# Kernel optimization log

Hardware: AMD Instinct MI355X
Metric: run time of the kernel (lower is better)

Reference implementation:

```python
import jax, jax.numpy as jnp
import numpy as np

B_SZ, SEQ, H, P = 4, 8192, 512, 256


def _s5(x, lam_re, lam_im, log_dt, b_re, b_im, c_re, c_im, d):
    """Single-direction S5 diagonal SSM. x: [B,L,H] -> y: [B,L,H]."""
    lam = lam_re + 1j * lam_im                      # [P] complex diagonal A
    dt = jnp.exp(log_dt)                            # [P] ZOH timestep
    a_bar = jnp.exp(lam * dt)                       # [P] discretized A
    b_bar = ((a_bar - 1.0) / lam)[:, None] * (b_re + 1j * b_im)  # [P,H]
    bu = jnp.einsum('blh,ph->blp', x.astype(b_bar.dtype), b_bar)  # [B,L,P]
    a_el = jnp.broadcast_to(a_bar, bu.shape)        # time-invariant A per step

    def comb(e1, e2):  # associative combine for linear recurrence
        a1, s1 = e1
        a2, s2 = e2
        return (a1 * a2, a2 * s1 + s2)

    _, states = jax.lax.associative_scan(comb, (a_el, bu), axis=1)  # [B,L,P]
    c = c_re + 1j * c_im                            # [H,P]
    return jnp.einsum('blp,hp->blh', states, c).real + x * d


def setup_inputs() -> dict:
    key = jax.random.key(0)
    ks = jax.random.split(key, 10)
    return {
        'x': jax.random.normal(ks[0], (B_SZ, SEQ, H), dtype=jnp.float32),
        'Lambda_re': -0.1 - 0.5 * jax.random.uniform(ks[1], (2, P), dtype=jnp.float32),
        'Lambda_im': jnp.pi * jax.random.normal(ks[2], (2, P), dtype=jnp.float32),
        'log_dt': jnp.log(0.001) + (jnp.log(0.1) - jnp.log(0.001)) * jax.random.uniform(ks[3], (2, P), dtype=jnp.float32),
        'B_re': jax.random.normal(ks[4], (2, P, H), dtype=jnp.float32) / np.sqrt(H),
        'B_im': jax.random.normal(ks[5], (2, P, H), dtype=jnp.float32) / np.sqrt(H),
        'C_re': jax.random.normal(ks[6], (2, H, P), dtype=jnp.float32) / np.sqrt(P),
        'C_im': jax.random.normal(ks[7], (2, H, P), dtype=jnp.float32) / np.sqrt(P),
        'D': jax.random.normal(ks[8], (2, H), dtype=jnp.float32),
    }


def reference(x, Lambda_re, Lambda_im, log_dt, B_re, B_im, C_re, C_im, D):
    # fwd(x) + flip(bwd(flip(x)))
    y_f = _s5(x, Lambda_re[0], Lambda_im[0], log_dt[0], B_re[0], B_im[0], C_re[0], C_im[0], D[0])
    x_r = x[:, ::-1]
    y_b = _s5(x_r, Lambda_re[1], Lambda_im[1], log_dt[1], B_re[1], B_im[1], C_re[1], C_im[1], D[1])[:, ::-1]
    return y_f + y_b
```

## Files before the change

### kernel.cpp

```cpp
#include <hip/hip_runtime.h>
#include <math.h>

typedef unsigned short ushort_t;
typedef __bf16 bf16x8 __attribute__((ext_vector_type(8)));
typedef ushort_t ushort8v __attribute__((ext_vector_type(8)));
typedef float f32x4 __attribute__((ext_vector_type(4)));

#define B_SZ   4
#define SEQ    8192
#define M_ROWS (B_SZ * SEQ)
#define CH     128
#define NC     (SEQ / CH)

__device__ __forceinline__ ushort_t f2bf(float f) {
    unsigned u = __float_as_uint(f);
    u = u + 0x7fffu + ((u >> 16) & 1u);
    return (ushort_t)(u >> 16);
}
__device__ __forceinline__ float bf2f(ushort_t b) {
    return __uint_as_float(((unsigned)b) << 16);
}

__device__ __forceinline__ void load16_lds(const void* g, void* l) {
    __builtin_amdgcn_global_load_lds(
        (const __attribute__((address_space(1))) unsigned int*)g,
        (__attribute__((address_space(3))) unsigned int*)l, 16, 0, 0);
}

__global__ void param_kernel(const float* __restrict__ Lre,
                             const float* __restrict__ Lim,
                             const float* __restrict__ ldt,
                             float* __restrict__ abar,
                             float* __restrict__ apow,
                             float* __restrict__ coef) {
    int d = blockIdx.x, p = threadIdx.x;
    int ip = d * 256 + p;
    float lr = Lre[ip], li = Lim[ip];
    float dt = expf(ldt[ip]);
    float e   = expf(lr * dt);
    float ang = li * dt;
    float ar = e * cosf(ang), ai = e * sinf(ang);
    float nr = ar - 1.0f, ni = ai;
    float den = lr * lr + li * li;
    float cr = (nr * lr + ni * li) / den;
    float ci = (ni * lr - nr * li) / den;
    int o = d * 512 + 2 * p;
    abar[o] = ar;  abar[o + 1] = ai;
    float eC = expf(lr * dt * (float)CH);
    float aC = ang * (float)CH;
    apow[o] = eC * cosf(aC);  apow[o + 1] = eC * sinf(aC);
    coef[o] = cr;  coef[o + 1] = ci;
}

__global__ void bmat_kernel(const float* __restrict__ Bre,
                            const float* __restrict__ Bim,
                            const float* __restrict__ coef,
                            ushort_t* __restrict__ Bmat) {
    int idx = blockIdx.x * 256 + threadIdx.x;
    int h = idx & 511;
    int p = (idx >> 9) & 255;
    int d = idx >> 17;
    float cr = coef[d * 512 + 2 * p], ci = coef[d * 512 + 2 * p + 1];
    float br = Bre[idx], bi = Bim[idx];
    Bmat[(d * 512 + p) * 512 + h]       = f2bf(cr * br - ci * bi);
    Bmat[(d * 512 + 256 + p) * 512 + h] = f2bf(cr * bi + ci * br);
}

__global__ void cmat_kernel(const float* __restrict__ Cre,
                            const float* __restrict__ Cim,
                            ushort_t* __restrict__ Cmat) {
    int idx = blockIdx.x * 256 + threadIdx.x;
    int p = idx & 255;
    int h = (idx >> 8) & 511;
    int d = idx >> 17;
    Cmat[(d * 512 + h) * 512 + p]       = f2bf(Cre[idx]);
    Cmat[(d * 512 + h) * 512 + 256 + p] = f2bf(-Cim[idx]);
}

__global__ void conv_x_kernel(const float* __restrict__ x,
                              ushort_t* __restrict__ X16) {
    int i = blockIdx.x * 256 + threadIdx.x;
    float4 v = ((const float4*)x)[i];
    ushort_t o[4] = {f2bf(v.x), f2bf(v.y), f2bf(v.z), f2bf(v.w)};
    *(uint2*)&X16[(size_t)i * 4] = *(const uint2*)o;
}

template<int EPI>
__global__ __launch_bounds__(256)
void gemm_mfma(const ushort_t* __restrict__ A, const ushort_t* __restrict__ Bm,
               ushort_t* __restrict__ Cb, float* __restrict__ Cf,
               const float* __restrict__ X, const float* __restrict__ Dv) {
    __shared__ ushort_t As[128 * 32];
    __shared__ ushort_t Bs[128 * 32];
    const int tid  = threadIdx.x;
    const int lane = tid & 63;
    const int wv   = tid >> 6;
    const int wrow = wv >> 1, wcol = wv & 1;
    const int l15  = lane & 15, lq = lane >> 4;
    const int m0 = blockIdx.y * 128;
    const int n0 = blockIdx.x * 128;

    f32x4 acc[4][4];
#pragma unroll
    for (int i = 0; i < 4; ++i)
#pragma unroll
        for (int j = 0; j < 4; ++j)
            acc[i][j] = (f32x4){0.f, 0.f, 0.f, 0.f};

    const int grow_l = lane >> 2;
    const int gk8    = (lane & 3) * 8;

    const ushort_t* aF = As + (wrow * 64 + l15) * 32 + lq * 8;
    const ushort_t* bF = Bs + (wcol * 64 + l15) * 32 + lq * 8;

    for (int kt = 0; kt < 512; kt += 32) {
        __syncthreads();
#pragma unroll
        for (int j = 0; j < 2; ++j) {
            const int r0 = j * 64 + wv * 16;
            load16_lds(&A[(size_t)(m0 + r0 + grow_l) * 512 + kt + gk8],
                       (void*)&As[r0 * 32]);
            load16_lds(&Bm[(size_t)(n0 + r0 + grow_l) * 512 + kt + gk8],
                       (void*)&Bs[r0 * 32]);
        }
        __syncthreads();

        bf16x8 af[4], bf[4];
#pragma unroll
        for (int mi = 0; mi < 4; ++mi) {
            union { ushort8v u; bf16x8 b; } cv;
            cv.u = *(const ushort8v*)(aF + mi * 512);
            af[mi] = cv.b;
        }
#pragma unroll
        for (int ni = 0; ni < 4; ++ni) {
            union { ushort8v u; bf16x8 b; } cv;
            cv.u = *(const ushort8v*)(bF + ni * 512);
            bf[ni] = cv.b;
        }
#pragma unroll
        for (int mi = 0; mi < 4; ++mi)
#pragma unroll
            for (int ni = 0; ni < 4; ++ni)
                acc[mi][ni] = __builtin_amdgcn_mfma_f32_16x16x32_bf16(
                    af[mi], bf[ni], acc[mi][ni], 0, 0, 0);
    }

#pragma unroll
    for (int mi = 0; mi < 4; ++mi) {
#pragma unroll
        for (int ni = 0; ni < 4; ++ni) {
            const int col = n0 + wcol * 64 + ni * 16 + l15;
            float dsum = 0.f;
            if (EPI == 1) dsum = Dv[col] + Dv[512 + col];
#pragma unroll
            for (int r = 0; r < 4; ++r) {
                const int row = m0 + wrow * 64 + mi * 16 + lq * 4 + r;
                const size_t idx = (size_t)row * 512 + col;
                float v = acc[mi][ni][r];
                if (EPI == 0) {
                    Cb[idx] = f2bf(v);
                } else if (EPI == 1) {
                    Cf[idx] = v + X[idx] * dsum;
                } else {
                    Cf[idx] += v;
                }
            }
        }
    }
}

template<int DIR>
__global__ __launch_bounds__(256)
void scan_carry(const ushort_t* __restrict__ S, const float* __restrict__ abar,
                float* __restrict__ carry) {
    int b = blockIdx.x, c = blockIdx.y, p = threadIdx.x;
    float ar = abar[2 * p], ai = abar[2 * p + 1];
    float sr = 0.f, si = 0.f;
    size_t base = ((size_t)b * SEQ + (size_t)c * CH) * 512;
    for (int ii = 0; ii < CH; ++ii) {
        int i = (DIR == 0) ? ii : (CH - 1 - ii);
        const ushort_t* r = S + base + (size_t)i * 512;
        float re = bf2f(r[p]), im = bf2f(r[256 + p]);
        float nr = fmaf(ar, sr, fmaf(-ai, si, re));
        float ni = fmaf(ar, si, fmaf(ai, sr, im));
        sr = nr; si = ni;
    }
    int o = (b * NC + c) * 512 + 2 * p;
    carry[o] = sr; carry[o + 1] = si;
}

template<int DIR>
__global__ void scan_comb(const float* __restrict__ carry,
                          float* __restrict__ init,
                          const float* __restrict__ apow) {
    int b = blockIdx.x, p = threadIdx.x;
    float pr = apow[2 * p], pi = apow[2 * p + 1];
    float sr = 0.f, si = 0.f;
    for (int cc = 0; cc < NC; ++cc) {
        int c = (DIR == 0) ? cc : (NC - 1 - cc);
        int o = (b * NC + c) * 512 + 2 * p;
        init[o] = sr; init[o + 1] = si;
        float cr = carry[o], ci = carry[o + 1];
        float nr = fmaf(pr, sr, fmaf(-pi, si, cr));
        float ni = fmaf(pr, si, fmaf(pi, sr, ci));
        sr = nr; si = ni;
    }
}

template<int DIR>
__global__ __launch_bounds__(256)
void scan_final(ushort_t* __restrict__ S, const float* __restrict__ abar,
                const float* __restrict__ init) {
    int b = blockIdx.x, c = blockIdx.y, p = threadIdx.x;
    float ar = abar[2 * p], ai = abar[2 * p + 1];
    int o = (b * NC + c) * 512 + 2 * p;
    float sr = init[o], si = init[o + 1];
    size_t base = ((size_t)b * SEQ + (size_t)c * CH) * 512;
    for (int ii = 0; ii < CH; ++ii) {
        int i = (DIR == 0) ? ii : (CH - 1 - ii);
        ushort_t* r = S + base + (size_t)i * 512;
        float re = bf2f(r[p]), im = bf2f(r[256 + p]);
        float nr = fmaf(ar, sr, fmaf(-ai, si, re));
        float ni = fmaf(ar, si, fmaf(ai, sr, im));
        sr = nr; si = ni;
        r[p] = f2bf(sr); r[256 + p] = f2bf(si);
    }
}

extern "C" void kernel_launch(void* const* d_in, const int* in_sizes, int n_in,
                              void* d_out, int out_size, void* d_ws, size_t ws_size,
                              hipStream_t stream) {
    const float* x   = (const float*)d_in[0];
    const float* Lre = (const float*)d_in[1];
    const float* Lim = (const float*)d_in[2];
    const float* ldt = (const float*)d_in[3];
    const float* Bre = (const float*)d_in[4];
    const float* Bim = (const float*)d_in[5];
    const float* Cre = (const float*)d_in[6];
    const float* Cim = (const float*)d_in[7];
    const float* Dv  = (const float*)d_in[8];
    float* y = (float*)d_out;
    char* ws = (char*)d_ws;

    ushort_t* X16  = (ushort_t*)(ws);
    ushort_t* SB16 = (ushort_t*)(ws + 33554432);
    ushort_t* Bm16 = (ushort_t*)(ws + 67108864);
    ushort_t* Cm16 = (ushort_t*)(ws + 68157440);
    float* abar  = (float*)(ws + 69206016);
    float* apow  = (float*)(ws + 69210112);
    float* coef  = (float*)(ws + 69214208);
    float* carry = (float*)(ws + 69218304);
    float* initb = (float*)(ws + 69742592);

    param_kernel<<<2, 256, 0, stream>>>(Lre, Lim, ldt, abar, apow, coef);
    bmat_kernel<<<1024, 256, 0, stream>>>(Bre, Bim, coef, Bm16);
    cmat_kernel<<<1024, 256, 0, stream>>>(Cre, Cim, Cm16);
    conv_x_kernel<<<16384, 256, 0, stream>>>(x, X16);

    dim3 gg(4, 256);
    dim3 gs(B_SZ, NC);

    gemm_mfma<0><<<gg, 256, 0, stream>>>(X16, Bm16, SB16, nullptr, nullptr, nullptr);
    scan_carry<0><<<gs, 256, 0, stream>>>(SB16, abar, carry);
    scan_comb<0><<<B_SZ, 256, 0, stream>>>(carry, initb, apow);
    scan_final<0><<<gs, 256, 0, stream>>>(SB16, abar, initb);
    gemm_mfma<1><<<gg, 256, 0, stream>>>(SB16, Cm16, nullptr, y, x, Dv);

    gemm_mfma<0><<<gg, 256, 0, stream>>>(X16, Bm16 + 262144, SB16, nullptr, nullptr, nullptr);
    scan_carry<1><<<gs, 256, 0, stream>>>(SB16, abar + 512, carry);
    scan_comb<1><<<B_SZ, 256, 0, stream>>>(carry, initb, apow + 512);
    scan_final<1><<<gs, 256, 0, stream>>>(SB16, abar + 512, initb);
    gemm_mfma<2><<<gg, 256, 0, stream>>>(SB16, Cm16 + 262144, nullptr, y, nullptr, nullptr);
}
```

Baseline: 328.9 us.

## Fuse both scan directions into single GEMM/scan passes with interleaved complex layout

Both directions now share one input-projection GEMM that produces an N=1024 interleaved re/im state matrix. Each scan kernel handles both directions with 512 threads, and a single K=1024 output GEMM replaces two output GEMMs plus the read-modify-write accumulation into y. The parameter, B-matrix and C-matrix prep kernels are merged into one, and GEMM blocks are remapped so that neighbouring M tiles land on the same XCD for L2 reuse. This removes launches, the second pass over x/y and the fp32 accumulate traffic, at the cost of a workspace twice as large and a reused carry/init region.

```diff
diff --git a/kernel.cpp b/kernel.cpp
--- a/kernel.cpp
+++ b/kernel.cpp
@@ -27,13 +27,21 @@
         (__attribute__((address_space(3))) unsigned int*)l, 16, 0, 0);
 }
 
-__global__ void param_kernel(const float* __restrict__ Lre,
-                             const float* __restrict__ Lim,
-                             const float* __restrict__ ldt,
-                             float* __restrict__ abar,
-                             float* __restrict__ apow,
-                             float* __restrict__ coef) {
-    int d = blockIdx.x, p = threadIdx.x;
+__global__ void prep_kernel(const float* __restrict__ Lre,
+                            const float* __restrict__ Lim,
+                            const float* __restrict__ ldt,
+                            const float* __restrict__ Bre,
+                            const float* __restrict__ Bim,
+                            const float* __restrict__ Cre,
+                            const float* __restrict__ Cim,
+                            float* __restrict__ abar,
+                            float* __restrict__ apow,
+                            ushort_t* __restrict__ Bmat,
+                            ushort_t* __restrict__ Cmat) {
+    int idx = blockIdx.x * 256 + threadIdx.x;
+    int h = idx & 511;
+    int p = (idx >> 9) & 255;
+    int d = idx >> 17;
     int ip = d * 256 + p;
     float lr = Lre[ip], li = Lim[ip];
     float dt = expf(ldt[ip]);
@@ -44,37 +52,21 @@
     float den = lr * lr + li * li;
     float cr = (nr * lr + ni * li) / den;
     float ci = (ni * lr - nr * li) / den;
-    int o = d * 512 + 2 * p;
-    abar[o] = ar;  abar[o + 1] = ai;
-    float eC = expf(lr * dt * (float)CH);
-    float aC = ang * (float)CH;
-    apow[o] = eC * cosf(aC);  apow[o + 1] = eC * sinf(aC);
-    coef[o] = cr;  coef[o + 1] = ci;
-}
-
-__global__ void bmat_kernel(const float* __restrict__ Bre,
-                            const float* __restrict__ Bim,
-                            const float* __restrict__ coef,
-                            ushort_t* __restrict__ Bmat) {
-    int idx = blockIdx.x * 256 + threadIdx.x;
-    int h = idx & 511;
-    int p = (idx >> 9) & 255;
-    int d = idx >> 17;
-    float cr = coef[d * 512 + 2 * p], ci = coef[d * 512 + 2 * p + 1];
     float br = Bre[idx], bi = Bim[idx];
-    Bmat[(d * 512 + p) * 512 + h]       = f2bf(cr * br - ci * bi);
-    Bmat[(d * 512 + 256 + p) * 512 + h] = f2bf(cr * bi + ci * br);
-}
-
-__global__ void cmat_kernel(const float* __restrict__ Cre,
-                            const float* __restrict__ Cim,
-                            ushort_t* __restrict__ Cmat) {
-    int idx = blockIdx.x * 256 + threadIdx.x;
-    int p = idx & 255;
-    int h = (idx >> 8) & 511;
-    int d = idx >> 17;
-    Cmat[(d * 512 + h) * 512 + p]       = f2bf(Cre[idx]);
-    Cmat[(d * 512 + h) * 512 + 256 + p] = f2bf(-Cim[idx]);
+    Bmat[(d * 512 + 2 * p) * 512 + h]     = f2bf(cr * br - ci * bi);
+    Bmat[(d * 512 + 2 * p + 1) * 512 + h] = f2bf(cr * bi + ci * br);
+    if (h == 0) {
+        int o = d * 512 + 2 * p;
+        abar[o] = ar;  abar[o + 1] = ai;
+        float eC = expf(lr * dt * (float)CH);
+        float aC = ang * (float)CH;
+        apow[o] = eC * cosf(aC);  apow[o + 1] = eC * sinf(aC);
+    }
+    int p2 = idx & 255;
+    int h2 = (idx >> 8) & 511;
+    int d2 = idx >> 17;
+    Cmat[h2 * 1024 + d2 * 512 + 2 * p2]     = f2bf(Cre[idx]);
+    Cmat[h2 * 1024 + d2 * 512 + 2 * p2 + 1] = f2bf(-Cim[idx]);
 }
 
 __global__ void conv_x_kernel(const float* __restrict__ x,
@@ -85,7 +77,7 @@
     *(uint2*)&X16[(size_t)i * 4] = *(const uint2*)o;
 }
 
-template<int EPI>
+template<int EPI, int KD_, int NT>
 __global__ __launch_bounds__(256)
 void gemm_mfma(const ushort_t* __restrict__ A, const ushort_t* __restrict__ Bm,
                ushort_t* __restrict__ Cb, float* __restrict__ Cf,
@@ -97,15 +89,22 @@
     const int wv   = tid >> 6;
     const int wrow = wv >> 1, wcol = wv & 1;
     const int l15  = lane & 15, lq = lane >> 4;
-    const int m0 = blockIdx.y * 128;
-    const int n0 = blockIdx.x * 128;
+
+    const int lin = blockIdx.x;
+    const int xcd = lin & 7;
+    const int j   = lin >> 3;
+    const int mt  = xcd * 32 + j / NT;
+    const int nt  = j % NT;
+    const int m0 = mt * 128;
+    const int n0 = nt * 128;
+    const int CN = NT * 128;
 
     f32x4 acc[4][4];
 #pragma unroll
     for (int i = 0; i < 4; ++i)
 #pragma unroll
-        for (int j = 0; j < 4; ++j)
-            acc[i][j] = (f32x4){0.f, 0.f, 0.f, 0.f};
+        for (int jj = 0; jj < 4; ++jj)
+            acc[i][jj] = (f32x4){0.f, 0.f, 0.f, 0.f};
 
     const int grow_l = lane >> 2;
     const int gk8    = (lane & 3) * 8;
@@ -113,19 +112,19 @@
     const ushort_t* aF = As + (wrow * 64 + l15) * 32 + lq * 8;
     const ushort_t* bF = Bs + (wcol * 64 + l15) * 32 + lq * 8;
 
-    for (int kt = 0; kt < 512; kt += 32) {
+    for (int kt = 0; kt < KD_; kt += 32) {
         __syncthreads();
 #pragma unroll
-        for (int j = 0; j < 2; ++j) {
-            const int r0 = j * 64 + wv * 16;
-            load16_lds(&A[(size_t)(m0 + r0 + grow_l) * 512 + kt + gk8],
+        for (int j2 = 0; j2 < 2; ++j2) {
+            const int r0 = j2 * 64 + wv * 16;
+            load16_lds(&A[(size_t)(m0 + r0 + grow_l) * KD_ + kt + gk8],
                        (void*)&As[r0 * 32]);
-            load16_lds(&Bm[(size_t)(n0 + r0 + grow_l) * 512 + kt + gk8],
+            load16_lds(&Bm[(size_t)(n0 + r0 + grow_l) * KD_ + kt + gk8],
                        (void*)&Bs[r0 * 32]);
         }
         __syncthreads();
 
-        bf16x8 af[4], bf[4];
+        bf16x8 af[4], bfr[4];
 #pragma unroll
         for (int mi = 0; mi < 4; ++mi) {
             union { ushort8v u; bf16x8 b; } cv;
@@ -136,14 +135,14 @@
         for (int ni = 0; ni < 4; ++ni) {
             union { ushort8v u; bf16x8 b; } cv;
             cv.u = *(const ushort8v*)(bF + ni * 512);
-            bf[ni] = cv.b;
+            bfr[ni] = cv.b;
         }
 #pragma unroll
         for (int mi = 0; mi < 4; ++mi)
 #pragma unroll
             for (int ni = 0; ni < 4; ++ni)
                 acc[mi][ni] = __builtin_amdgcn_mfma_f32_16x16x32_bf16(
-                    af[mi], bf[ni], acc[mi][ni], 0, 0, 0);
+                    af[mi], bfr[ni], acc[mi][ni], 0, 0, 0);
     }
 
 #pragma unroll
@@ -156,50 +155,49 @@
 #pragma unroll
             for (int r = 0; r < 4; ++r) {
                 const int row = m0 + wrow * 64 + mi * 16 + lq * 4 + r;
-                const size_t idx = (size_t)row * 512 + col;
-                float v = acc[mi][ni][r];
                 if (EPI == 0) {
-                    Cb[idx] = f2bf(v);
-                } else if (EPI == 1) {
-                    Cf[idx] = v + X[idx] * dsum;
+                    Cb[(size_t)row * CN + col] = f2bf(acc[mi][ni][r]);
                 } else {
-                    Cf[idx] += v;
+                    const size_t idx = (size_t)row * 512 + col;
+                    Cf[idx] = acc[mi][ni][r] + X[idx] * dsum;
                 }
             }
         }
     }
 }
 
-template<int DIR>
-__global__ __launch_bounds__(256)
+__global__ __launch_bounds__(512)
 void scan_carry(const ushort_t* __restrict__ S, const float* __restrict__ abar,
                 float* __restrict__ carry) {
-    int b = blockIdx.x, c = blockIdx.y, p = threadIdx.x;
-    float ar = abar[2 * p], ai = abar[2 * p + 1];
+    int b = blockIdx.x, c = blockIdx.y, t = threadIdx.x;
+    int dir = t >> 8, p = t & 255;
+    float ar = abar[dir * 512 + 2 * p], ai = abar[dir * 512 + 2 * p + 1];
     float sr = 0.f, si = 0.f;
-    size_t base = ((size_t)b * SEQ + (size_t)c * CH) * 512;
+    const ushort_t* base = S + ((size_t)b * SEQ + (size_t)c * CH) * 1024
+                             + dir * 512 + 2 * p;
     for (int ii = 0; ii < CH; ++ii) {
-        int i = (DIR == 0) ? ii : (CH - 1 - ii);
-        const ushort_t* r = S + base + (size_t)i * 512;
-        float re = bf2f(r[p]), im = bf2f(r[256 + p]);
+        int i = dir ? (CH - 1 - ii) : ii;
+        unsigned u = *(const unsigned*)(base + (size_t)i * 1024);
+        float re = bf2f((ushort_t)(u & 0xffffu));
+        float im = bf2f((ushort_t)(u >> 16));
         float nr = fmaf(ar, sr, fmaf(-ai, si, re));
         float ni = fmaf(ar, si, fmaf(ai, sr, im));
         sr = nr; si = ni;
     }
-    int o = (b * NC + c) * 512 + 2 * p;
+    int o = (b * NC + c) * 1024 + dir * 512 + 2 * p;
     carry[o] = sr; carry[o + 1] = si;
 }
 
-template<int DIR>
-__global__ void scan_comb(const float* __restrict__ carry,
-                          float* __restrict__ init,
-                          const float* __restrict__ apow) {
-    int b = blockIdx.x, p = threadIdx.x;
-    float pr = apow[2 * p], pi = apow[2 * p + 1];
+__global__ __launch_bounds__(512)
+void scan_comb(const float* __restrict__ carry, float* __restrict__ init,
+               const float* __restrict__ apow) {
+    int b = blockIdx.x, t = threadIdx.x;
+    int dir = t >> 8, p = t & 255;
+    float pr = apow[dir * 512 + 2 * p], pi = apow[dir * 512 + 2 * p + 1];
     float sr = 0.f, si = 0.f;
     for (int cc = 0; cc < NC; ++cc) {
-        int c = (DIR == 0) ? cc : (NC - 1 - cc);
-        int o = (b * NC + c) * 512 + 2 * p;
+        int c = dir ? (NC - 1 - cc) : cc;
+        int o = (b * NC + c) * 1024 + dir * 512 + 2 * p;
         init[o] = sr; init[o + 1] = si;
         float cr = carry[o], ci = carry[o + 1];
         float nr = fmaf(pr, sr, fmaf(-pi, si, cr));
@@ -208,23 +206,26 @@
     }
 }
 
-template<int DIR>
-__global__ __launch_bounds__(256)
+__global__ __launch_bounds__(512)
 void scan_final(ushort_t* __restrict__ S, const float* __restrict__ abar,
                 const float* __restrict__ init) {
-    int b = blockIdx.x, c = blockIdx.y, p = threadIdx.x;
-    float ar = abar[2 * p], ai = abar[2 * p + 1];
-    int o = (b * NC + c) * 512 + 2 * p;
+    int b = blockIdx.x, c = blockIdx.y, t = threadIdx.x;
+    int dir = t >> 8, p = t & 255;
+    float ar = abar[dir * 512 + 2 * p], ai = abar[dir * 512 + 2 * p + 1];
+    int o = (b * NC + c) * 1024 + dir * 512 + 2 * p;
     float sr = init[o], si = init[o + 1];
-    size_t base = ((size_t)b * SEQ + (size_t)c * CH) * 512;
+    ushort_t* base = S + ((size_t)b * SEQ + (size_t)c * CH) * 1024
+                       + dir * 512 + 2 * p;
     for (int ii = 0; ii < CH; ++ii) {
-        int i = (DIR == 0) ? ii : (CH - 1 - ii);
-        ushort_t* r = S + base + (size_t)i * 512;
-        float re = bf2f(r[p]), im = bf2f(r[256 + p]);
+        int i = dir ? (CH - 1 - ii) : ii;
+        unsigned* addr = (unsigned*)(base + (size_t)i * 1024);
+        unsigned u = *addr;
+        float re = bf2f((ushort_t)(u & 0xffffu));
+        float im = bf2f((ushort_t)(u >> 16));
         float nr = fmaf(ar, sr, fmaf(-ai, si, re));
         float ni = fmaf(ar, si, fmaf(ai, sr, im));
         sr = nr; si = ni;
-        r[p] = f2bf(sr); r[256 + p] = f2bf(si);
+        *addr = ((unsigned)f2bf(si) << 16) | (unsigned)f2bf(sr);
     }
 }
 
@@ -243,33 +244,27 @@
     float* y = (float*)d_out;
     char* ws = (char*)d_ws;
 
-    ushort_t* X16  = (ushort_t*)(ws);
-    ushort_t* SB16 = (ushort_t*)(ws + 33554432);
-    ushort_t* Bm16 = (ushort_t*)(ws + 67108864);
-    ushort_t* Cm16 = (ushort_t*)(ws + 68157440);
-    float* abar  = (float*)(ws + 69206016);
-    float* apow  = (float*)(ws + 69210112);
-    float* coef  = (float*)(ws + 69214208);
-    float* carry = (float*)(ws + 69218304);
-    float* initb = (float*)(ws + 69742592);
-
-    param_kernel<<<2, 256, 0, stream>>>(Lre, Lim, ldt, abar, apow, coef);
-    bmat_kernel<<<1024, 256, 0, stream>>>(Bre, Bim, coef, Bm16);
-    cmat_kernel<<<1024, 256, 0, stream>>>(Cre, Cim, Cm16);
+    ushort_t* SB16 = (ushort_t*)(ws);
+    ushort_t* X16  = (ushort_t*)(ws + 67108864);
+    ushort_t* Bm16 = (ushort_t*)(ws + 100663296);
+    ushort_t* Cm16 = (ushort_t*)(ws + 101711872);
+    float* abar  = (float*)(ws + 102760448);
+    float* apow  = (float*)(ws + 102764544);
+    float* carry = (float*)(ws + 67108864);
+    float* initb = (float*)(ws + 68157440);
+
+    prep_kernel<<<1024, 256, 0, stream>>>(Lre, Lim, ldt, Bre, Bim, Cre, Cim,
+                                          abar, apow, Bm16, Cm16);
     conv_x_kernel<<<16384, 256, 0, stream>>>(x, X16);
 
-    dim3 gg(4, 256);
+    gemm_mfma<0, 512, 8><<<2048, 256, 0, stream>>>(X16, Bm16, SB16, nullptr,
+                                                   nullptr, nullptr);
+
     dim3 gs(B_SZ, NC);
-
-    gemm_mfma<0><<<gg, 256, 0, stream>>>(X16, Bm16, SB16, nullptr, nullptr, nullptr);
-    scan_carry<0><<<gs, 256, 0, stream>>>(SB16, abar, carry);
-    scan_comb<0><<<B_SZ, 256, 0, stream>>>(carry, initb, apow);
-    scan_final<0><<<gs, 256, 0, stream>>>(SB16, abar, initb);
-    gemm_mfma<1><<<gg, 256, 0, stream>>>(SB16, Cm16, nullptr, y, x, Dv);
-
-    gemm_mfma<0><<<gg, 256, 0, stream>>>(X16, Bm16 + 262144, SB16, nullptr, nullptr, nullptr);
-    scan_carry<1><<<gs, 256, 0, stream>>>(SB16, abar + 512, carry);
-    scan_comb<1><<<B_SZ, 256, 0, stream>>>(carry, initb, apow + 512);
-    scan_final<1><<<gs, 256, 0, stream>>>(SB16, abar + 512, initb);
-    gemm_mfma<2><<<gg, 256, 0, stream>>>(SB16, Cm16 + 262144, nullptr, y, nullptr, nullptr);
-}
+    scan_carry<<<gs, 512, 0, stream>>>(SB16, abar, carry);
+    scan_comb<<<B_SZ, 512, 0, stream>>>(carry, initb, apow);
+    scan_final<<<gs, 512, 0, stream>>>(SB16, abar, initb);
+
+    gemm_mfma<1, 1024, 4><<<1024, 256, 0, stream>>>(SB16, Cm16, nullptr, y,
+                                                    x, Dv);
+}
```

After: 286.9 us. 12.8% less time.
